# Performance work log

Hardware: AMD Instinct MI355X
Metric: run time of the kernel (lower is better)

## Reference

```python
import jax, jax.numpy as jnp
import numpy as np

E = 4_194_304
N_COMPANY = 100_000
N_CAUSE, N_COURT, N_RES = 200, 50, 10
D_CA, D_COURT, D_CATE = 12, 4, 4
D = D_CA + D_COURT + D_CATE  # 20


def setup_inputs() -> dict:
    key = jax.random.key(0)
    ks = jax.random.split(key, 10)
    cause_idx = jax.random.randint(ks[0], (E,), 0, N_CAUSE, dtype=jnp.int32)
    court_idx = jax.random.randint(ks[1], (E,), 0, N_COURT, dtype=jnp.int32)
    cate_idx = jax.random.randint(ks[2], (E,), 0, N_RES, dtype=jnp.int32)
    seg_ids = jnp.sort(jax.random.randint(ks[3], (E,), 0, N_COMPANY, dtype=jnp.int32))
    time_interval = jax.random.uniform(ks[4], (E,), dtype=jnp.float32) * 365.0
    # learned parameters (nn.Embedding default init ~ N(0,1); Linear ~ U)
    ca_table = jax.random.normal(ks[5], (N_CAUSE, D_CA), dtype=jnp.float32)
    court_table = jax.random.normal(ks[6], (N_COURT, D_COURT), dtype=jnp.float32)
    cate_table = jax.random.normal(ks[7], (N_RES, D_CATE), dtype=jnp.float32)
    lim = 1.0 / np.sqrt(D)
    proj_w = jax.random.uniform(ks[8], (D, D), dtype=jnp.float32, minval=-lim, maxval=lim)
    decay_w = jax.random.uniform(ks[9], (), dtype=jnp.float32, minval=0.5, maxval=1.5)
    return {
        "cause_idx": cause_idx, "court_idx": court_idx, "cate_idx": cate_idx,
        "seg_ids": seg_ids, "time_interval": time_interval,
        "ca_table": ca_table, "court_table": court_table, "cate_table": cate_table,
        "proj_w": proj_w, "decay_w": decay_w,
    }


def reference(cause_idx, court_idx, cate_idx, seg_ids, time_interval,
              ca_table, court_table, cate_table, proj_w, decay_w):
    # per-event categorical embedding gather -> [E, 20]
    risk = jnp.concatenate(
        [ca_table[cause_idx], court_table[court_idx], cate_table[cate_idx]], axis=1)
    # Decayer: learnable scale times inverse-log time decay
    decay = decay_w / jnp.log(jnp.e + time_interval)  # [E]
    # proj(decay * risk): Linear(20, 20, bias=False) -> x @ W^T
    y = jnp.einsum('ed,od->eo', decay[:, None] * risk, proj_w)
    # per-company sum reduction (the original Python loop over companies)
    com_emb = jax.ops.segment_sum(y, seg_ids, num_segments=N_COMPANY,
                                  indices_are_sorted=True)
    return com_emb
```

## Files before the change

kernel.cpp:

```cpp
#include <hip/hip_runtime.h>

#define NCOMP   100000
#define D_CA    12
#define D_COURT 4
#define D_CATE  4
#define D_TOT   20
#define NCAUSE  200
#define NCOURT  50
#define NRES    10
#define LPC     8
#define CPB     32

__global__ __launch_bounds__(256)
void fused_company_kernel(const int* __restrict__ cause_idx,
                          const int* __restrict__ court_idx,
                          const int* __restrict__ cate_idx,
                          const int* __restrict__ seg_ids,
                          const float* __restrict__ time_interval,
                          const float* __restrict__ ca_table,
                          const float* __restrict__ court_table,
                          const float* __restrict__ cate_table,
                          const float* __restrict__ proj_w,
                          const float* __restrict__ decay_w,
                          int n_events,
                          float* __restrict__ out) {
    __shared__ __align__(16) float lds_ca[NCAUSE * D_CA];
    __shared__ __align__(16) float lds_court[NCOURT * D_COURT];
    __shared__ __align__(16) float lds_cate[NRES * D_CATE];
    __shared__ __align__(16) float lds_w[D_TOT * D_TOT];
    __shared__ int lds_start[CPB + 1];

    for (int i = threadIdx.x; i < NCAUSE * D_CA; i += 256) lds_ca[i] = ca_table[i];
    for (int i = threadIdx.x; i < NCOURT * D_COURT; i += 256) lds_court[i] = court_table[i];
    for (int i = threadIdx.x; i < NRES * D_CATE; i += 256) lds_cate[i] = cate_table[i];
    for (int i = threadIdx.x; i < D_TOT * D_TOT; i += 256) lds_w[i] = proj_w[i];

    if (threadIdx.x <= CPB) {
        const int c = blockIdx.x * CPB + threadIdx.x;
        int lo = 0, hi = n_events;
        while (lo < hi) {
            const int mid = (lo + hi) >> 1;
            if (seg_ids[mid] < c) lo = mid + 1; else hi = mid;
        }
        lds_start[threadIdx.x] = lo;
    }
    __syncthreads();

    const float dw = decay_w[0];
    const int g   = threadIdx.x >> 3;
    const int sub = threadIdx.x & (LPC - 1);
    const int c   = blockIdx.x * CPB + g;
    const int s0  = lds_start[g];
    const int s1  = lds_start[g + 1];

    float acc[D_TOT];
#pragma unroll
    for (int d = 0; d < D_TOT; ++d) acc[d] = 0.0f;

#define EV_BODY(I)                                                           \
    {                                                                        \
        const int   ca = cause_idx[I];                                       \
        const int   co = court_idx[I];                                       \
        const int   ct = cate_idx[I];                                        \
        const float t  = time_interval[I];                                   \
        const float dec = __fdividef(dw, __logf(2.718281828459045f + t));    \
        const float4* car = (const float4*)(lds_ca + ca * D_CA);             \
        const float4 a0 = car[0];                                            \
        const float4 a1 = car[1];                                            \
        const float4 a2 = car[2];                                            \
        const float4 b0 = *(const float4*)(lds_court + co * D_COURT);        \
        const float4 c0 = *(const float4*)(lds_cate + ct * D_CATE);          \
        acc[0]  += dec * a0.x;  acc[1]  += dec * a0.y;                       \
        acc[2]  += dec * a0.z;  acc[3]  += dec * a0.w;                       \
        acc[4]  += dec * a1.x;  acc[5]  += dec * a1.y;                       \
        acc[6]  += dec * a1.z;  acc[7]  += dec * a1.w;                       \
        acc[8]  += dec * a2.x;  acc[9]  += dec * a2.y;                       \
        acc[10] += dec * a2.z;  acc[11] += dec * a2.w;                       \
        acc[12] += dec * b0.x;  acc[13] += dec * b0.y;                       \
        acc[14] += dec * b0.z;  acc[15] += dec * b0.w;                       \
        acc[16] += dec * c0.x;  acc[17] += dec * c0.y;                       \
        acc[18] += dec * c0.z;  acc[19] += dec * c0.w;                       \
    }

    int i = s0 + sub;
    for (; i + LPC < s1; i += 2 * LPC) {
        EV_BODY(i);
        EV_BODY(i + LPC);
    }
    if (i < s1) EV_BODY(i);
#undef EV_BODY

#pragma unroll
    for (int d = 0; d < D_TOT; ++d) {
        float v = acc[d];
        v += __shfl_xor(v, 1);
        v += __shfl_xor(v, 2);
        v += __shfl_xor(v, 4);
        acc[d] = v;
    }

    for (int o = sub; o < D_TOT; o += LPC) {
        float s = 0.0f;
#pragma unroll
        for (int d = 0; d < D_TOT; ++d) s += acc[d] * lds_w[o * D_TOT + d];
        out[c * D_TOT + o] = s;
    }
}

extern "C" void kernel_launch(void* const* d_in, const int* in_sizes, int n_in,
                              void* d_out, int out_size, void* d_ws, size_t ws_size,
                              hipStream_t stream) {
    const int* cause_idx = (const int*)d_in[0];
    const int* court_idx = (const int*)d_in[1];
    const int* cate_idx  = (const int*)d_in[2];
    const int* seg_ids   = (const int*)d_in[3];
    const float* time_interval = (const float*)d_in[4];
    const float* ca_table      = (const float*)d_in[5];
    const float* court_table   = (const float*)d_in[6];
    const float* cate_table    = (const float*)d_in[7];
    const float* proj_w        = (const float*)d_in[8];
    const float* decay_w       = (const float*)d_in[9];
    float* out = (float*)d_out;
    const int n_events = in_sizes[0];

    const int blocks = NCOMP / CPB;
    fused_company_kernel<<<blocks, 256, 0, stream>>>(
        cause_idx, court_idx, cate_idx, seg_ids, time_interval,
        ca_table, court_table, cate_table, proj_w, decay_w,
        n_events, out);
}
```

Before: 148.9 us.

## Switch to event-parallel chunked reduction with atomic per-segment outputs

Replaces the company-per-group kernel, which used a binary search per company and 8 lanes per segment, with one thread per 16 consecutive events. Each thread loads its inputs as vector int4/float4, keeps head and tail accumulators, applies the projection, and atomically adds into an output zeroed by a memset. Chunks spanning more than two segments fall back to a scalar slow path. This aims to balance load and make loads coalesced, at the cost of many float atomics and an extra memset launch.

```diff
diff --git a/kernel.cpp b/kernel.cpp
--- a/kernel.cpp
+++ b/kernel.cpp
@@ -8,102 +8,183 @@
 #define NCAUSE  200
 #define NCOURT  50
 #define NRES    10
-#define LPC     8
-#define CPB     32
-
-__global__ __launch_bounds__(256)
-void fused_company_kernel(const int* __restrict__ cause_idx,
-                          const int* __restrict__ court_idx,
-                          const int* __restrict__ cate_idx,
-                          const int* __restrict__ seg_ids,
-                          const float* __restrict__ time_interval,
-                          const float* __restrict__ ca_table,
-                          const float* __restrict__ court_table,
-                          const float* __restrict__ cate_table,
-                          const float* __restrict__ proj_w,
-                          const float* __restrict__ decay_w,
-                          int n_events,
-                          float* __restrict__ out) {
+#define CHUNK   16
+
+__device__ __forceinline__ void slow_chunk(long base, int jmax, float dw,
+                                           const int* __restrict__ cause_idx,
+                                           const int* __restrict__ court_idx,
+                                           const int* __restrict__ cate_idx,
+                                           const int* __restrict__ seg_ids,
+                                           const float* __restrict__ time_interval,
+                                           const float* lds_ca, const float* lds_court,
+                                           const float* lds_cate, const float* lds_w,
+                                           float* __restrict__ out) {
+    float acc[D_TOT];
+#pragma unroll 1
+    for (int d = 0; d < D_TOT; ++d) acc[d] = 0.0f;
+    int cur = seg_ids[base];
+#pragma unroll 1
+    for (int j = 0; j < jmax; ++j) {
+        const int sj = seg_ids[base + j];
+        if (sj != cur) {
+#pragma unroll 1
+            for (int o = 0; o < D_TOT; ++o) {
+                float s = 0.0f;
+#pragma unroll 1
+                for (int d = 0; d < D_TOT; ++d) s += acc[d] * lds_w[o * D_TOT + d];
+                atomicAdd(&out[cur * D_TOT + o], s);
+            }
+#pragma unroll 1
+            for (int d = 0; d < D_TOT; ++d) acc[d] = 0.0f;
+            cur = sj;
+        }
+        const int ca = cause_idx[base + j];
+        const int co = court_idx[base + j];
+        const int ct = cate_idx[base + j];
+        const float t = time_interval[base + j];
+        const float dec = __fdividef(dw, __logf(2.718281828459045f + t));
+#pragma unroll 1
+        for (int d = 0; d < D_CA; ++d) acc[d] += dec * lds_ca[ca * D_CA + d];
+#pragma unroll 1
+        for (int d = 0; d < D_COURT; ++d) acc[D_CA + d] += dec * lds_court[co * D_COURT + d];
+#pragma unroll 1
+        for (int d = 0; d < D_CATE; ++d) acc[D_CA + D_COURT + d] += dec * lds_cate[ct * D_CATE + d];
+    }
+#pragma unroll 1
+    for (int o = 0; o < D_TOT; ++o) {
+        float s = 0.0f;
+#pragma unroll 1
+        for (int d = 0; d < D_TOT; ++d) s += acc[d] * lds_w[o * D_TOT + d];
+        atomicAdd(&out[cur * D_TOT + o], s);
+    }
+}
+
+__global__ __launch_bounds__(256, 4)
+void event_sum_kernel(const int* __restrict__ cause_idx,
+                      const int* __restrict__ court_idx,
+                      const int* __restrict__ cate_idx,
+                      const int* __restrict__ seg_ids,
+                      const float* __restrict__ time_interval,
+                      const float* __restrict__ ca_table,
+                      const float* __restrict__ court_table,
+                      const float* __restrict__ cate_table,
+                      const float* __restrict__ proj_w,
+                      const float* __restrict__ decay_w,
+                      int n_events,
+                      float* __restrict__ out) {
     __shared__ __align__(16) float lds_ca[NCAUSE * D_CA];
     __shared__ __align__(16) float lds_court[NCOURT * D_COURT];
     __shared__ __align__(16) float lds_cate[NRES * D_CATE];
     __shared__ __align__(16) float lds_w[D_TOT * D_TOT];
-    __shared__ int lds_start[CPB + 1];
 
     for (int i = threadIdx.x; i < NCAUSE * D_CA; i += 256) lds_ca[i] = ca_table[i];
     for (int i = threadIdx.x; i < NCOURT * D_COURT; i += 256) lds_court[i] = court_table[i];
     for (int i = threadIdx.x; i < NRES * D_CATE; i += 256) lds_cate[i] = cate_table[i];
     for (int i = threadIdx.x; i < D_TOT * D_TOT; i += 256) lds_w[i] = proj_w[i];
-
-    if (threadIdx.x <= CPB) {
-        const int c = blockIdx.x * CPB + threadIdx.x;
-        int lo = 0, hi = n_events;
-        while (lo < hi) {
-            const int mid = (lo + hi) >> 1;
-            if (seg_ids[mid] < c) lo = mid + 1; else hi = mid;
+    __syncthreads();
+
+    const float dw = decay_w[0];
+    const int tid = blockIdx.x * 256 + threadIdx.x;
+    const long base = (long)tid * CHUNK;
+    if (base >= n_events) return;
+
+    if (base + CHUNK > n_events) {
+        slow_chunk(base, (int)(n_events - base), dw, cause_idx, court_idx, cate_idx,
+                   seg_ids, time_interval, lds_ca, lds_court, lds_cate, lds_w, out);
+        return;
+    }
+
+    const int4* seg4 = (const int4*)(seg_ids + base);
+    const int4 s0 = seg4[0], s1 = seg4[1], s2 = seg4[2], s3 = seg4[3];
+    const int first = s0.x, last = s3.w;
+
+    const bool slow =
+        ((s0.y != first) & (s0.y != last)) | ((s0.z != first) & (s0.z != last)) |
+        ((s0.w != first) & (s0.w != last)) | ((s1.x != first) & (s1.x != last)) |
+        ((s1.y != first) & (s1.y != last)) | ((s1.z != first) & (s1.z != last)) |
+        ((s1.w != first) & (s1.w != last)) | ((s2.x != first) & (s2.x != last)) |
+        ((s2.y != first) & (s2.y != last)) | ((s2.z != first) & (s2.z != last)) |
+        ((s2.w != first) & (s2.w != last)) | ((s3.x != first) & (s3.x != last)) |
+        ((s3.y != first) & (s3.y != last)) | ((s3.z != first) & (s3.z != last));
+
+    if (slow) {
+        slow_chunk(base, CHUNK, dw, cause_idx, court_idx, cate_idx,
+                   seg_ids, time_interval, lds_ca, lds_court, lds_cate, lds_w, out);
+        return;
+    }
+
+    const int4* ca4 = (const int4*)(cause_idx + base);
+    const int4* co4 = (const int4*)(court_idx + base);
+    const int4* ct4 = (const int4*)(cate_idx + base);
+    const float4* tm4 = (const float4*)(time_interval + base);
+
+    float accH[D_TOT], accT[D_TOT];
+#pragma unroll
+    for (int d = 0; d < D_TOT; ++d) { accH[d] = 0.0f; accT[d] = 0.0f; }
+
+#define PROC(CA, CO, CT, T, S)                                                \
+    do {                                                                      \
+        const float dec  = __fdividef(dw, __logf(2.718281828459045f + (T)));  \
+        const float decT = ((S) != first) ? dec : 0.0f;                       \
+        const float decH = dec - decT;                                        \
+        const float4* car = (const float4*)(lds_ca + (CA) * D_CA);            \
+        const float4 a0 = car[0], a1 = car[1], a2 = car[2];                   \
+        const float4 b0 = *(const float4*)(lds_court + (CO) * D_COURT);       \
+        const float4 c0 = *(const float4*)(lds_cate + (CT) * D_CATE);         \
+        accH[0]  += decH * a0.x;  accT[0]  += decT * a0.x;                    \
+        accH[1]  += decH * a0.y;  accT[1]  += decT * a0.y;                    \
+        accH[2]  += decH * a0.z;  accT[2]  += decT * a0.z;                    \
+        accH[3]  += decH * a0.w;  accT[3]  += decT * a0.w;                    \
+        accH[4]  += decH * a1.x;  accT[4]  += decT * a1.x;                    \
+        accH[5]  += decH * a1.y;  accT[5]  += decT * a1.y;                    \
+        accH[6]  += decH * a1.z;  accT[6]  += decT * a1.z;                    \
+        accH[7]  += decH * a1.w;  accT[7]  += decT * a1.w;                    \
+        accH[8]  += decH * a2.x;  accT[8]  += decT * a2.x;                    \
+        accH[9]  += decH * a2.y;  accT[9]  += decT * a2.y;                    \
+        accH[10] += decH * a2.z;  accT[10] += decT * a2.z;                    \
+        accH[11] += decH * a2.w;  accT[11] += decT * a2.w;                    \
+        accH[12] += decH * b0.x;  accT[12] += decT * b0.x;                    \
+        accH[13] += decH * b0.y;  accT[13] += decT * b0.y;                    \
+        accH[14] += decH * b0.z;  accT[14] += decT * b0.z;                    \
+        accH[15] += decH * b0.w;  accT[15] += decT * b0.w;                    \
+        accH[16] += decH * c0.x;  accT[16] += decT * c0.x;                    \
+        accH[17] += decH * c0.y;  accT[17] += decT * c0.y;                    \
+        accH[18] += decH * c0.z;  accT[18] += decT * c0.z;                    \
+        accH[19] += decH * c0.w;  accT[19] += decT * c0.w;                    \
+    } while (0)
+
+#define GROUP(J, SV)                                                          \
+    do {                                                                      \
+        const int4 ca = ca4[J]; const int4 co = co4[J];                       \
+        const int4 ct = ct4[J]; const float4 tm = tm4[J];                     \
+        PROC(ca.x, co.x, ct.x, tm.x, SV.x);                                   \
+        PROC(ca.y, co.y, ct.y, tm.y, SV.y);                                   \
+        PROC(ca.z, co.z, ct.z, tm.z, SV.z);                                   \
+        PROC(ca.w, co.w, ct.w, tm.w, SV.w);                                   \
+    } while (0)
+
+    GROUP(0, s0);
+    GROUP(1, s1);
+    GROUP(2, s2);
+    GROUP(3, s3);
+#undef GROUP
+#undef PROC
+
+#pragma unroll
+    for (int o = 0; o < D_TOT; ++o) {
+        float s = 0.0f;
+#pragma unroll
+        for (int d = 0; d < D_TOT; ++d) s += accH[d] * lds_w[o * D_TOT + d];
+        atomicAdd(&out[first * D_TOT + o], s);
+    }
+    if (last != first) {
+#pragma unroll
+        for (int o = 0; o < D_TOT; ++o) {
+            float s = 0.0f;
+#pragma unroll
+            for (int d = 0; d < D_TOT; ++d) s += accT[d] * lds_w[o * D_TOT + d];
+            atomicAdd(&out[last * D_TOT + o], s);
         }
-        lds_start[threadIdx.x] = lo;
-    }
-    __syncthreads();
-
-    const float dw = decay_w[0];
-    const int g   = threadIdx.x >> 3;
-    const int sub = threadIdx.x & (LPC - 1);
-    const int c   = blockIdx.x * CPB + g;
-    const int s0  = lds_start[g];
-    const int s1  = lds_start[g + 1];
-
-    float acc[D_TOT];
-#pragma unroll
-    for (int d = 0; d < D_TOT; ++d) acc[d] = 0.0f;
-
-#define EV_BODY(I)                                                           \
-    {                                                                        \
-        const int   ca = cause_idx[I];                                       \
-        const int   co = court_idx[I];                                       \
-        const int   ct = cate_idx[I];                                        \
-        const float t  = time_interval[I];                                   \
-        const float dec = __fdividef(dw, __logf(2.718281828459045f + t));    \
-        const float4* car = (const float4*)(lds_ca + ca * D_CA);             \
-        const float4 a0 = car[0];                                            \
-        const float4 a1 = car[1];                                            \
-        const float4 a2 = car[2];                                            \
-        const float4 b0 = *(const float4*)(lds_court + co * D_COURT);        \
-        const float4 c0 = *(const float4*)(lds_cate + ct * D_CATE);          \
-        acc[0]  += dec * a0.x;  acc[1]  += dec * a0.y;                       \
-        acc[2]  += dec * a0.z;  acc[3]  += dec * a0.w;                       \
-        acc[4]  += dec * a1.x;  acc[5]  += dec * a1.y;                       \
-        acc[6]  += dec * a1.z;  acc[7]  += dec * a1.w;                       \
-        acc[8]  += dec * a2.x;  acc[9]  += dec * a2.y;                       \
-        acc[10] += dec * a2.z;  acc[11] += dec * a2.w;                       \
-        acc[12] += dec * b0.x;  acc[13] += dec * b0.y;                       \
-        acc[14] += dec * b0.z;  acc[15] += dec * b0.w;                       \
-        acc[16] += dec * c0.x;  acc[17] += dec * c0.y;                       \
-        acc[18] += dec * c0.z;  acc[19] += dec * c0.w;                       \
-    }
-
-    int i = s0 + sub;
-    for (; i + LPC < s1; i += 2 * LPC) {
-        EV_BODY(i);
-        EV_BODY(i + LPC);
-    }
-    if (i < s1) EV_BODY(i);
-#undef EV_BODY
-
-#pragma unroll
-    for (int d = 0; d < D_TOT; ++d) {
-        float v = acc[d];
-        v += __shfl_xor(v, 1);
-        v += __shfl_xor(v, 2);
-        v += __shfl_xor(v, 4);
-        acc[d] = v;
-    }
-
-    for (int o = sub; o < D_TOT; o += LPC) {
-        float s = 0.0f;
-#pragma unroll
-        for (int d = 0; d < D_TOT; ++d) s += acc[d] * lds_w[o * D_TOT + d];
-        out[c * D_TOT + o] = s;
     }
 }
 
@@ -123,8 +204,11 @@
     float* out = (float*)d_out;
     const int n_events = in_sizes[0];
 
-    const int blocks = NCOMP / CPB;
-    fused_company_kernel<<<blocks, 256, 0, stream>>>(
+    hipMemsetAsync(out, 0, (size_t)out_size * sizeof(float), stream);
+
+    const int threads_total = (n_events + CHUNK - 1) / CHUNK;
+    const int blocks = (threads_total + 255) / 256;
+    event_sum_kernel<<<blocks, 256, 0, stream>>>(
         cause_idx, court_idx, cate_idx, seg_ids, time_interval,
         ca_table, court_table, cate_table, proj_w, decay_w,
         n_events, out);
```

Result: slower. 521.6 us (+250.3%).
